# Optimization experiments

Measured on AMD Instinct MI355X. Metric: run time of the kernel, lower is better.

The kernel has to match this reference:

```python
import jax, jax.numpy as jnp
import numpy as np

DIRECTIONAL_WEIGHT = 0.85
MAGNITUDE_WEIGHT = 0.15
TREND_WEIGHT = 0.1
EPS = 1e-8

B = 8388608
C = 3


def setup_inputs() -> dict:
    key = jax.random.key(0)
    k1, k2, k3, k4 = jax.random.split(key, 4)
    predictions = jax.random.normal(k1, (B, C), dtype=jnp.float32)
    targets = jax.random.randint(k2, (B,), 0, C, dtype=jnp.int32)
    price_changes = jax.random.normal(k3, (B,), dtype=jnp.float32)
    trend_direction = jax.random.normal(k4, (B,), dtype=jnp.float32)
    return {
        "predictions": predictions,
        "targets": targets,
        "price_changes": price_changes,
        "trend_direction": trend_direction,
    }


def reference(predictions, targets, price_changes, trend_direction):
    # per-sample cross entropy (reduction='none')
    logp = jax.nn.log_softmax(predictions, axis=1)  # [B, C]
    ce_loss = -jnp.take_along_axis(logp, targets[:, None].astype(jnp.int32), axis=1)[:, 0]  # [B]

    # magnitude weighting
    magnitude_weights = jnp.abs(price_changes)
    magnitude_weights = magnitude_weights / (magnitude_weights.mean() + EPS)
    weighted_ce = ce_loss * magnitude_weights

    # vectorized trend alignment (replaces the python loop)
    up_aligned = (trend_direction > 0) & (targets == 2)
    down_aligned = (trend_direction < 0) & (targets == 0)
    trend_alignment = jnp.where(up_aligned | down_aligned, -0.1, 0.0).astype(ce_loss.dtype)

    total_loss = (
        DIRECTIONAL_WEIGHT * weighted_ce.mean()
        + MAGNITUDE_WEIGHT * ce_loss.mean()
        + TREND_WEIGHT * trend_alignment.mean()
    )
    return total_loss
```

## Files before the change

kernel.cpp:

```cpp
#include <hip/hip_runtime.h>

#define B_TOTAL 8388608

__global__ __launch_bounds__(256) void trading_loss_main(
    const float* __restrict__ preds,
    const int*   __restrict__ targets,
    const float* __restrict__ pc,
    const float* __restrict__ td,
    float* __restrict__ sums,
    int nquads)
{
    float s_cew = 0.f, s_ce = 0.f, s_mw = 0.f, s_tr = 0.f;

    int tid = blockIdx.x * blockDim.x + threadIdx.x;
    int stride = gridDim.x * blockDim.x;

    for (int q = tid; q < nquads; q += stride) {
        const float4* p4 = reinterpret_cast<const float4*>(preds + (size_t)q * 12);
        float4 a = p4[0];
        float4 b = p4[1];
        float4 c = p4[2];
        float p[12] = {a.x,a.y,a.z,a.w, b.x,b.y,b.z,b.w, c.x,c.y,c.z,c.w};

        int4   t4  = reinterpret_cast<const int4*  >(targets)[q];
        float4 pc4 = reinterpret_cast<const float4*>(pc)[q];
        float4 td4 = reinterpret_cast<const float4*>(td)[q];
        int   tt[4]  = {t4.x, t4.y, t4.z, t4.w};
        float pcv[4] = {pc4.x, pc4.y, pc4.z, pc4.w};
        float tdv[4] = {td4.x, td4.y, td4.z, td4.w};

        #pragma unroll
        for (int j = 0; j < 4; ++j) {
            float p0 = p[j*3 + 0], p1 = p[j*3 + 1], p2 = p[j*3 + 2];
            float m  = fmaxf(fmaxf(p0, p1), p2);
            float e0 = __expf(p0 - m);
            float e1 = __expf(p1 - m);
            float e2 = __expf(p2 - m);
            float lse = __logf(e0 + e1 + e2);
            int   t  = tt[j];
            float pt = (t == 0) ? p0 : ((t == 1) ? p1 : p2);
            float ce = lse - (pt - m);
            float aw = fabsf(pcv[j]);

            s_ce  += ce;
            s_cew += ce * aw;
            s_mw  += aw;
            bool aligned = (tdv[j] > 0.f && t == 2) || (tdv[j] < 0.f && t == 0);
            s_tr += aligned ? 1.0f : 0.0f;
        }
    }

    #pragma unroll
    for (int off = 32; off >= 1; off >>= 1) {
        s_cew += __shfl_down(s_cew, off, 64);
        s_ce  += __shfl_down(s_ce , off, 64);
        s_mw  += __shfl_down(s_mw , off, 64);
        s_tr  += __shfl_down(s_tr , off, 64);
    }

    __shared__ float red[4][4];
    int lane = threadIdx.x & 63;
    int wave = threadIdx.x >> 6;
    if (lane == 0) {
        red[wave][0] = s_cew;
        red[wave][1] = s_ce;
        red[wave][2] = s_mw;
        red[wave][3] = s_tr;
    }
    __syncthreads();

    if (threadIdx.x == 0) {
        float r0 = 0.f, r1 = 0.f, r2 = 0.f, r3 = 0.f;
        #pragma unroll
        for (int w = 0; w < 4; ++w) {
            r0 += red[w][0]; r1 += red[w][1]; r2 += red[w][2]; r3 += red[w][3];
        }
        atomicAdd(&sums[0], r0);
        atomicAdd(&sums[1], r1);
        atomicAdd(&sums[2], r2);
        atomicAdd(&sums[3], r3);
    }
}

__global__ void trading_loss_final(const float* __restrict__ sums,
                                   float* __restrict__ out)
{
    const float invB = 1.0f / (float)B_TOTAL;
    float cew_mean = sums[0] * invB;
    float ce_mean  = sums[1] * invB;
    float mw_mean  = sums[2] * invB + 1e-8f;
    float tr_mean  = -0.1f * sums[3] * invB;
    out[0] = 0.85f * (cew_mean / mw_mean) + 0.15f * ce_mean + 0.1f * tr_mean;
}

extern "C" void kernel_launch(void* const* d_in, const int* in_sizes, int n_in,
                              void* d_out, int out_size, void* d_ws, size_t ws_size,
                              hipStream_t stream) {
    const float* preds   = (const float*)d_in[0];
    const int*   targets = (const int*  )d_in[1];
    const float* pc      = (const float*)d_in[2];
    const float* td      = (const float*)d_in[3];
    float* out  = (float*)d_out;
    float* sums = (float*)d_ws;

    hipMemsetAsync(sums, 0, 4 * sizeof(float), stream);

    int nquads = in_sizes[1] / 4;

    trading_loss_main<<<2048, 256, 0, stream>>>(preds, targets, pc, td, sums, nquads);
    trading_loss_final<<<1, 1, 0, stream>>>(sums, out);
}
```

Baseline: 277.7 us.

## Fuse finalize into main kernel and batch all loads up front

Replaces the grid-stride loop with a compile-time unrolled loop in which every thread issues all of its vector loads (4 quads) before any compute, so more memory requests are in flight at once. The separate single-thread finalize kernel is removed: the last block to finish, detected with an atomic counter, computes the output. This saves one kernel launch and raises memory-level parallelism, at the cost of more registers and of hardcoding the problem size.

New measurement: 328.0 us. +18.1%, slower.

```diff
diff --git a/kernel.cpp b/kernel.cpp
--- a/kernel.cpp
+++ b/kernel.cpp
@@ -1,33 +1,53 @@
 #include <hip/hip_runtime.h>
 
-#define B_TOTAL 8388608
+#define B_TOTAL   8388608
+#define NQUADS    (B_TOTAL / 4)
+#define THREADS   256
+#define BLOCKS    2048
+#define NTHREADS  (BLOCKS * THREADS)
+#define UNROLL    (NQUADS / NTHREADS)
 
-__global__ __launch_bounds__(256) void trading_loss_main(
+__global__ __launch_bounds__(THREADS, 4) void trading_loss_fused(
     const float* __restrict__ preds,
     const int*   __restrict__ targets,
     const float* __restrict__ pc,
     const float* __restrict__ td,
-    float* __restrict__ sums,
-    int nquads)
+    float*        __restrict__ sums,
+    unsigned int* __restrict__ count,
+    float*        __restrict__ out)
 {
+    const unsigned tid = blockIdx.x * THREADS + threadIdx.x;
+
+    const float4* preds4 = reinterpret_cast<const float4*>(preds);
+    const int4*   tg4    = reinterpret_cast<const int4*  >(targets);
+    const float4* pc4    = reinterpret_cast<const float4*>(pc);
+    const float4* td4    = reinterpret_cast<const float4*>(td);
+
+    float4 A0[UNROLL], A1[UNROLL], A2[UNROLL];
+    int4   T[UNROLL];
+    float4 P[UNROLL], D[UNROLL];
+
+    #pragma unroll
+    for (int u = 0; u < UNROLL; ++u) {
+        const unsigned q = u * NTHREADS + tid;
+        A0[u] = preds4[(size_t)q * 3 + 0];
+        A1[u] = preds4[(size_t)q * 3 + 1];
+        A2[u] = preds4[(size_t)q * 3 + 2];
+        T[u]  = tg4[q];
+        P[u]  = pc4[q];
+        D[u]  = td4[q];
+    }
+
     float s_cew = 0.f, s_ce = 0.f, s_mw = 0.f, s_tr = 0.f;
 
-    int tid = blockIdx.x * blockDim.x + threadIdx.x;
-    int stride = gridDim.x * blockDim.x;
-
-    for (int q = tid; q < nquads; q += stride) {
-        const float4* p4 = reinterpret_cast<const float4*>(preds + (size_t)q * 12);
-        float4 a = p4[0];
-        float4 b = p4[1];
-        float4 c = p4[2];
-        float p[12] = {a.x,a.y,a.z,a.w, b.x,b.y,b.z,b.w, c.x,c.y,c.z,c.w};
-
-        int4   t4  = reinterpret_cast<const int4*  >(targets)[q];
-        float4 pc4 = reinterpret_cast<const float4*>(pc)[q];
-        float4 td4 = reinterpret_cast<const float4*>(td)[q];
-        int   tt[4]  = {t4.x, t4.y, t4.z, t4.w};
-        float pcv[4] = {pc4.x, pc4.y, pc4.z, pc4.w};
-        float tdv[4] = {td4.x, td4.y, td4.z, td4.w};
+    #pragma unroll
+    for (int u = 0; u < UNROLL; ++u) {
+        float p[12] = {A0[u].x, A0[u].y, A0[u].z, A0[u].w,
+                       A1[u].x, A1[u].y, A1[u].z, A1[u].w,
+                       A2[u].x, A2[u].y, A2[u].z, A2[u].w};
+        int   tt[4]  = {T[u].x, T[u].y, T[u].z, T[u].w};
+        float pcv[4] = {P[u].x, P[u].y, P[u].z, P[u].w};
+        float tdv[4] = {D[u].x, D[u].y, D[u].z, D[u].w};
 
         #pragma unroll
         for (int j = 0; j < 4; ++j) {
@@ -59,8 +79,8 @@
     }
 
     __shared__ float red[4][4];
-    int lane = threadIdx.x & 63;
-    int wave = threadIdx.x >> 6;
+    const int lane = threadIdx.x & 63;
+    const int wave = threadIdx.x >> 6;
     if (lane == 0) {
         red[wave][0] = s_cew;
         red[wave][1] = s_ce;
@@ -70,27 +90,32 @@
     __syncthreads();
 
     if (threadIdx.x == 0) {
-        float r0 = 0.f, r1 = 0.f, r2 = 0.f, r3 = 0.f;
-        #pragma unroll
-        for (int w = 0; w < 4; ++w) {
-            r0 += red[w][0]; r1 += red[w][1]; r2 += red[w][2]; r3 += red[w][3];
-        }
+        float r0 = red[0][0] + red[1][0] + red[2][0] + red[3][0];
+        float r1 = red[0][1] + red[1][1] + red[2][1] + red[3][1];
+        float r2 = red[0][2] + red[1][2] + red[2][2] + red[3][2];
+        float r3 = red[0][3] + red[1][3] + red[2][3] + red[3][3];
+
         atomicAdd(&sums[0], r0);
         atomicAdd(&sums[1], r1);
         atomicAdd(&sums[2], r2);
         atomicAdd(&sums[3], r3);
+
+        __threadfence();
+        unsigned old = atomicAdd(count, 1u);
+        if (old == BLOCKS - 1) {
+            float cew = atomicAdd(&sums[0], 0.0f);
+            float ce  = atomicAdd(&sums[1], 0.0f);
+            float mw  = atomicAdd(&sums[2], 0.0f);
+            float tr  = atomicAdd(&sums[3], 0.0f);
+
+            const float invB = 1.0f / (float)B_TOTAL;
+            float cew_mean = cew * invB;
+            float ce_mean  = ce  * invB;
+            float mw_mean  = mw  * invB + 1e-8f;
+            float tr_mean  = -0.1f * tr * invB;
+            out[0] = 0.85f * (cew_mean / mw_mean) + 0.15f * ce_mean + 0.1f * tr_mean;
+        }
     }
-}
-
-__global__ void trading_loss_final(const float* __restrict__ sums,
-                                   float* __restrict__ out)
-{
-    const float invB = 1.0f / (float)B_TOTAL;
-    float cew_mean = sums[0] * invB;
-    float ce_mean  = sums[1] * invB;
-    float mw_mean  = sums[2] * invB + 1e-8f;
-    float tr_mean  = -0.1f * sums[3] * invB;
-    out[0] = 0.85f * (cew_mean / mw_mean) + 0.15f * ce_mean + 0.1f * tr_mean;
 }
 
 extern "C" void kernel_launch(void* const* d_in, const int* in_sizes, int n_in,
@@ -102,11 +127,10 @@
     const float* td      = (const float*)d_in[3];
     float* out  = (float*)d_out;
     float* sums = (float*)d_ws;
+    unsigned int* count = (unsigned int*)((char*)d_ws + 4 * sizeof(float));
 
-    hipMemsetAsync(sums, 0, 4 * sizeof(float), stream);
+    hipMemsetAsync(d_ws, 0, 5 * sizeof(float), stream);
 
-    int nquads = in_sizes[1] / 4;
-
-    trading_loss_main<<<2048, 256, 0, stream>>>(preds, targets, pc, td, sums, nquads);
-    trading_loss_final<<<1, 1, 0, stream>>>(sums, out);
+    trading_loss_fused<<<BLOCKS, THREADS, 0, stream>>>(preds, targets, pc, td,
+                                                       sums, count, out);
 }
```
